# Kernel optimization log

Hardware: AMD Instinct MI355X
Metric: run time of the kernel (lower is better)

The kernel has to match this reference:

```python
import jax, jax.numpy as jnp
import numpy as np


def setup_inputs() -> dict:
    key = jax.random.key(0)
    ks = jax.random.split(key, 10)
    N, S, H = 500000, 128, 64
    s = lambda k, shape, fan_in: jax.random.normal(k, shape, dtype=jnp.float32) / np.sqrt(fan_in)
    return {
        "my_state": jax.random.normal(ks[0], (S,), dtype=jnp.float32),
        "neighbor_states": jax.random.normal(ks[1], (N, S), dtype=jnp.float32),
        "embed_w": s(ks[2], (S, H), S),
        "embed_b": s(ks[3], (H,), S),
        "key_w": s(ks[4], (H, H), H),
        "key_b": s(ks[5], (H,), H),
        "query_w": s(ks[6], (S + H, H), S + H),
        "query_b": s(ks[7], (H,), S + H),
        "attn_w": s(ks[8], (2 * H, 1), 2 * H),
        "attn_b": s(ks[9], (1,), 2 * H),
    }


def reference(my_state, neighbor_states, embed_w, embed_b, key_w, key_b,
              query_w, query_b, attn_w, attn_b):
    H = embed_w.shape[1]
    # per-neighbor embeddings and keys: [N, H]
    emb = neighbor_states @ embed_w + embed_b
    keys = emb @ key_w + key_b
    # query from own state + mean neighbor embedding: [H]
    mean_emb = emb.mean(axis=0)
    query = jnp.concatenate([my_state, mean_emb], axis=-1) @ query_w + query_b
    # attention_net(cat(query, key)) split so we never materialize [N, 2H]
    wq, wk = attn_w[:H, 0], attn_w[H:, 0]
    scores = keys @ wk + (query @ wq + attn_b[0])  # [N]
    attention_weights = jax.nn.softmax(scores, axis=0)  # [N]
    weighted_embedding = attention_weights @ emb  # [H]
    return weighted_embedding, attention_weights
```

## Files before the change

### kernel.cpp

```cpp
#include <hip/hip_runtime.h>
#include <math.h>


#define S_DIM 128
#define H_DIM 64
#define NBLK  2048
#define NB2   512

typedef float f4 __attribute__((ext_vector_type(4)));

__global__ __launch_bounds__(256) void k_stream(
    const float* __restrict__ X,
    const float* __restrict__ embed_w,
    const float* __restrict__ key_w,
    const float* __restrict__ attn_w,
    float* __restrict__ e_out,
    float* __restrict__ pz,
    float* __restrict__ pv_t,
    int N)
{
    __shared__ float s_kv[H_DIM];
    __shared__ float s_u[S_DIM];
    __shared__ float sT[8][S_DIM];
    __shared__ float sZ[8];
    __shared__ float red[256];

    const int tid = threadIdx.x;

    if (tid < H_DIM) {
        float acc = 0.f;
        #pragma unroll 8
        for (int j = 0; j < H_DIM; ++j) acc += key_w[tid * H_DIM + j] * attn_w[H_DIM + j];
        s_kv[tid] = acc;
    }
    __syncthreads();
    if (tid < S_DIM) {
        float acc = 0.f;
        #pragma unroll 8
        for (int h = 0; h < H_DIM; ++h) acc += embed_w[tid * H_DIM + h] * s_kv[h];
        s_u[tid] = acc;
    }
    __syncthreads();

    const int lane = tid & 63;
    const int li   = lane & 31;
    const int half = lane >> 5;
    const int w    = tid >> 6;

    const f4 u4 = *(const f4*)(s_u + 4 * li);

    const int pairs = (N + 1) >> 1;
    const int start = (int)(((long long)blockIdx.x       * pairs) / NBLK);
    const int end   = (int)(((long long)(blockIdx.x + 1) * pairs) / NBLK);

    auto loadp = [&](int p) -> f4 {
        int row = 2 * p + half;
        row = row < N ? row : N - 1;
        return *(const f4*)(X + (size_t)row * S_DIM + 4 * li);
    };

    float Za = 0.f, Zb = 0.f;
    f4 ta = (f4)(0.f), tb = (f4)(0.f);

    auto proc = [&](const f4& x, int p, float& Z, f4& t) {
        float pp = x.x * u4.x + x.y * u4.y + x.z * u4.z + x.w * u4.w;
        pp += __shfl_xor(pp, 1);
        pp += __shfl_xor(pp, 2);
        pp += __shfl_xor(pp, 4);
        pp += __shfl_xor(pp, 8);
        pp += __shfl_xor(pp, 16);
        const int  row = 2 * p + half;
        const bool v   = (p < end) && (row < N);
        const float e  = v ? __expf(pp) : 0.f;
        if (li == 0 && v) e_out[row] = e;
        Z += e;
        t += e * x;
    };

    int p = start + w;
    f4 xa = loadp(p);
    f4 xb = loadp(p + 4);
    while (p < end) {
        f4 na = loadp(p + 8);
        f4 nb = loadp(p + 12);
        proc(xa, p,     Za, ta);
        proc(xb, p + 4, Zb, tb);
        xa = na; xb = nb; p += 8;
    }

    const float Z = Za + Zb;
    const f4    t = ta + tb;

    const int hs = w * 2 + half;
    *(f4*)(&sT[hs][4 * li]) = t;
    if (li == 0) sZ[hs] = Z;
    __syncthreads();

    if (tid < S_DIM)
        s_u[tid] = sT[0][tid] + sT[1][tid] + sT[2][tid] + sT[3][tid]
                 + sT[4][tid] + sT[5][tid] + sT[6][tid] + sT[7][tid];
    if (tid == 0)
        pz[blockIdx.x] = sZ[0] + sZ[1] + sZ[2] + sZ[3] + sZ[4] + sZ[5] + sZ[6] + sZ[7];
    __syncthreads();

    {
        const int h = tid & 63, q4 = tid >> 6;
        float acc = 0.f;
        #pragma unroll 8
        for (int k = 32 * q4; k < 32 * q4 + 32; ++k)
            acc += s_u[k] * embed_w[k * H_DIM + h];
        red[tid] = acc;
        __syncthreads();
        if (tid < H_DIM)
            pv_t[(size_t)tid * NBLK + blockIdx.x] =
                red[tid] + red[tid + 64] + red[tid + 128] + red[tid + 192];
    }
}

__global__ __launch_bounds__(256) void k_final(
    float* __restrict__ sw,
    const float* __restrict__ pz,
    const float* __restrict__ pv_t,
    const float* __restrict__ embed_b,
    float* __restrict__ out_emb,
    int N)
{
    __shared__ float red[256];
    const int tid = threadIdx.x;
    const int bid = blockIdx.x;

    float z = 0.f;
    for (int i = tid; i < NBLK; i += 256) z += pz[i];
    red[tid] = z; __syncthreads();
    for (int s = 128; s; s >>= 1) { if (tid < s) red[tid] += red[tid + s]; __syncthreads(); }
    const float invZ = 1.0f / red[0];
    __syncthreads();

    const int n4 = N >> 2;
    for (int i = bid * 256 + tid; i < n4; i += NB2 * 256) {
        f4 v = ((f4*)sw)[i];
        v *= invZ;
        ((f4*)sw)[i] = v;
    }
    if (bid == 0 && tid == 0)
        for (int i = n4 << 2; i < N; ++i) sw[i] *= invZ;

    if (bid < H_DIM) {
        float a = 0.f;
        for (int i = tid; i < NBLK; i += 256) a += pv_t[(size_t)bid * NBLK + i];
        red[tid] = a; __syncthreads();
        for (int s = 128; s; s >>= 1) { if (tid < s) red[tid] += red[tid + s]; __syncthreads(); }
        if (tid == 0) out_emb[bid] = red[0] * invZ + embed_b[bid];
    }
}

extern "C" void kernel_launch(void* const* d_in, const int* in_sizes, int n_in,
                              void* d_out, int out_size, void* d_ws, size_t ws_size,
                              hipStream_t stream) {
    const float* X       = (const float*)d_in[1];
    const float* embed_w = (const float*)d_in[2];
    const float* embed_b = (const float*)d_in[3];
    const float* key_w   = (const float*)d_in[4];
    const float* attn_w  = (const float*)d_in[8];
    float* out = (float*)d_out;

    const int N = in_sizes[1] / S_DIM;

    float* pz   = (float*)d_ws;
    float* pv_t = pz + NBLK;

    float* out_emb = out;
    float* out_w   = out + H_DIM;

    k_stream<<<NBLK, 256, 0, stream>>>(X, embed_w, key_w, attn_w, out_w, pz, pv_t, N);
    k_final<<<NB2, 256, 0, stream>>>(out_w, pz, pv_t, embed_b, out_emb, N);
}
```

Baseline: 63.83 us.

## Use grid-strided wave scheduling with four-deep load prefetch in stream kernel

Rows are no longer split into contiguous per-block chunks. Each wave now walks row pairs with a grid-wide stride, so all waves together sweep memory in order. The software prefetch depth doubles from two to four outstanding 512-byte row-pair loads per wave, to keep more bytes in flight and hide HBM latency. The cost is more live registers, and per-block locality gives way to interleaved access across the whole grid.

New measurement: 70.71 us. 10.8% more time.

```diff
diff --git a/kernel.cpp b/kernel.cpp
--- a/kernel.cpp
+++ b/kernel.cpp
@@ -50,8 +50,8 @@
     const f4 u4 = *(const f4*)(s_u + 4 * li);
 
     const int pairs = (N + 1) >> 1;
-    const int start = (int)(((long long)blockIdx.x       * pairs) / NBLK);
-    const int end   = (int)(((long long)(blockIdx.x + 1) * pairs) / NBLK);
+    const int gw    = blockIdx.x * 4 + w;
+    const int W     = NBLK * 4;
 
     auto loadp = [&](int p) -> f4 {
         int row = 2 * p + half;
@@ -70,22 +70,30 @@
         pp += __shfl_xor(pp, 8);
         pp += __shfl_xor(pp, 16);
         const int  row = 2 * p + half;
-        const bool v   = (p < end) && (row < N);
+        const bool v   = (p < pairs) && (row < N);
         const float e  = v ? __expf(pp) : 0.f;
         if (li == 0 && v) e_out[row] = e;
         Z += e;
         t += e * x;
     };
 
-    int p = start + w;
-    f4 xa = loadp(p);
-    f4 xb = loadp(p + 4);
-    while (p < end) {
-        f4 na = loadp(p + 8);
-        f4 nb = loadp(p + 12);
-        proc(xa, p,     Za, ta);
-        proc(xb, p + 4, Zb, tb);
-        xa = na; xb = nb; p += 8;
+    int p = gw;
+    f4 x0 = loadp(p);
+    f4 x1 = loadp(p + W);
+    f4 x2 = loadp(p + 2 * W);
+    f4 x3 = loadp(p + 3 * W);
+
+    while (p < pairs) {
+        f4 n0 = loadp(p + 4 * W);
+        f4 n1 = loadp(p + 5 * W);
+        f4 n2 = loadp(p + 6 * W);
+        f4 n3 = loadp(p + 7 * W);
+        proc(x0, p,         Za, ta);
+        proc(x1, p + W,     Zb, tb);
+        proc(x2, p + 2 * W, Za, ta);
+        proc(x3, p + 3 * W, Zb, tb);
+        x0 = n0; x1 = n1; x2 = n2; x3 = n3;
+        p += 4 * W;
     }
 
     const float Z = Za + Zb;
```
